# Performance work log

Hardware: AMD Instinct MI355X
Metric: run time of the kernel (lower is better)

The kernel has to match this reference:

```python
import jax, jax.numpy as jnp
import numpy as np
from jax import lax

B, CIN, COUT, H, W, K = 32, 256, 256, 56, 56, 3

def setup_inputs() -> dict:
    key = jax.random.key(0)
    k1, k2, k3 = jax.random.split(key, 3)
    inp = jax.random.normal(k1, (B, CIN, H, W), dtype=jnp.float32)
    # kaiming-style init for conv kernel, normal init for bias
    fan_in = CIN * K * K
    kernel = jax.random.normal(k2, (COUT, CIN, K, K), dtype=jnp.float32) * np.float32(np.sqrt(2.0 / fan_in))
    bias = jax.random.normal(k3, (COUT,), dtype=jnp.float32)
    return {"inp": inp, "kernel": kernel, "bias": bias}

def reference(inp, kernel, bias):
    # Equivalent to the crossbar path: im2col 3x3 patches @ stacked [kernel|bias]
    # matrix == standard conv2d(padding=1, stride=1) + bias.
    out = lax.conv_general_dilated(
        inp, kernel,
        window_strides=(1, 1),
        padding=((1, 1), (1, 1)),
        dimension_numbers=("NCHW", "OIHW", "NCHW"),
    )
    return out + bias[None, :, None, None]
```

## Files before the change

kernel.cpp:

```cpp
#include <hip/hip_runtime.h>
#include <hip/hip_bf16.h>


#define BB    32
#define CINC  256
#define COUTC 256
#define HH    56
#define WW    56
#define HP    58
#define WP    58
#define PIX_PER_IMG 3136
#define NPIX  100352
#define KTOT  2304
#define NKT   72

#define XT_BYTES ((size_t)BB*HP*WP*CINC*2)
#define AWR_FRAGS (72*16*64)
#define AWR_BYTES ((size_t)AWR_FRAGS*16)

#define RING   4096
#define WLDS   (3*RING)

using frag_t = __attribute__((ext_vector_type(8))) short;
using f32x4  = __attribute__((ext_vector_type(4))) float;

__device__ __forceinline__ void gload_lds16(const void* gsrc, void* ldst) {
  __builtin_amdgcn_global_load_lds(
      (const __attribute__((address_space(1))) unsigned*)gsrc,
      (__attribute__((address_space(3))) unsigned*)ldst, 16, 0, 0);
}

__global__ void xpose_kernel(const float* __restrict__ inp,
                             __hip_bfloat16* __restrict__ xt) {
  int bid = blockIdx.x;
  int hp = bid % HP;
  int t  = bid / HP;
  int cb = t % 4;
  int b  = t / 4;
  __shared__ __hip_bfloat16 tile[64 * 60];
  int tid = threadIdx.x;
  for (int i = tid; i < 64 * 60; i += 256) tile[i] = __float2bfloat16(0.f);
  __syncthreads();
  int h = hp - 1;
  if (h >= 0 && h < HH) {
    const float* src = inp + ((size_t)(b * CINC + cb * 64) * HH + h) * WW;
    for (int i = tid; i < 64 * WW; i += 256) {
      int ci = i / WW, w = i - ci * WW;
      tile[ci * 60 + (w + 1)] = __float2bfloat16(src[(size_t)ci * HH * WW + w]);
    }
  }
  __syncthreads();
  __hip_bfloat16* dst = xt + ((size_t)(b * HP + hp) * WP) * CINC + cb * 64;
  for (int i = tid; i < WP * 64; i += 256) {
    int wp = i >> 6, ci = i & 63;
    dst[(size_t)wp * CINC + ci] = tile[ci * 60 + wp];
  }
}

__global__ void wprep_pack(const float* __restrict__ k4,
                           frag_t* __restrict__ awr) {
  int i = blockIdx.x * 256 + threadIdx.x;
  if (i >= AWR_FRAGS) return;
  int lane = i & 63;
  int mb   = (i >> 6) & 15;
  int t    = i >> 10;
  int co   = mb * 16 + (lane & 15);
  int kb   = t * 32 + (lane >> 4) * 8;
  frag_t v;
#pragma unroll
  for (int j = 0; j < 8; ++j) {
    int k = kb + j;
    int tap = k >> 8;
    int ci  = k & 255;
    __hip_bfloat16 h = __float2bfloat16(k4[(co * CINC + ci) * 9 + tap]);
    v[j] = *reinterpret_cast<short*>(&h);
  }
  awr[i] = v;
}

__global__ __launch_bounds__(256, 3) void conv_free(
    const __hip_bfloat16* __restrict__ xt,
    const frag_t* __restrict__ awr,
    const float* __restrict__ bias,
    float* __restrict__ out) {
  __shared__ alignas(16) char lds[4 * WLDS];

  const int tid  = threadIdx.x;
  const int lane = tid & 63;
  const int wid  = tid >> 6;
  const int wm   = wid >> 1;
  const int wn   = wid & 1;
  const int fr   = lane & 15;
  const int g    = lane >> 4;

  const int bid   = blockIdx.x;
  const int wgid  = (bid & 7) * 196 + (bid >> 3);
  const int ctile = wgid & 1;
  const int ptile = wgid >> 1;

  const char* xt_b = (const char*)xt;
  char* wbase = lds + wid * WLDS;

  const int lr  = lane >> 2;
  const int sc  = ((((lane & 3) - ((lane >> 3) & 3)) & 3) << 4);

  auto mkB = [&](int jb) -> const char* {
    int px = ptile * 128 + wn * 64 + jb * 16 + lr;
    int b  = px / PIX_PER_IMG;
    int hw = px - b * PIX_PER_IMG;
    int h = hw / WW, w = hw - h * WW;
    return xt_b + (size_t)((b * HP + h) * WP + w) * (CINC * 2) + sc;
  };
  const char* pB0 = mkB(0);
  const char* pB1 = mkB(1);
  const char* pB2 = mkB(2);
  const char* pB3 = mkB(3);

#define STG(T2, WB) {                                                      \
    int _tap = (T2) >> 3; int _rr = _tap / 3, _ss = _tap - _rr * 3;        \
    size_t _bo = (size_t)(_rr * WP + _ss) * (CINC * 2)                     \
               + (size_t)((T2) & 7) * 64;                                  \
    char* _d = wbase + (WB) * RING;                                        \
    gload_lds16(pB0 + _bo, _d + 0);                                        \
    gload_lds16(pB1 + _bo, _d + 1024);                                     \
    gload_lds16(pB2 + _bo, _d + 2048);                                     \
    gload_lds16(pB3 + _bo, _d + 3072); }

  const frag_t* abase = awr + (size_t)(ctile * 8 + wm * 4) * 64 + lane;

#define ALOAD(T1, FA) {                                                    \
    const frag_t* _p = abase + (size_t)(T1) * (16 * 64);                   \
    _Pragma("unroll") for (int m = 0; m < 4; ++m)                          \
      FA[m] = _p[m * 64]; }

  const int ckr   = (((g + (fr >> 1)) & 3) << 4);
  const int broff = fr * 64 + ckr;

  frag_t fa0[4], fa1[4], fb[4];
  f32x4 acc[4][4] = {};

#define RSL(RB) {                                                          \
    const char* _b = wbase + (RB) * RING;                                  \
    _Pragma("unroll") for (int n = 0; n < 4; ++n)                          \
      fb[n] = *(const frag_t*)(_b + broff + n * 1024); }

#define MF(FA) {                                                           \
    __builtin_amdgcn_s_setprio(1);                                         \
    _Pragma("unroll") for (int m = 0; m < 4; ++m)                          \
    _Pragma("unroll") for (int n = 0; n < 4; ++n)                          \
      acc[m][n] = __builtin_amdgcn_mfma_f32_16x16x32_bf16(                 \
          FA[m], fb[n], acc[m][n], 0, 0, 0);                               \
    __builtin_amdgcn_s_setprio(0); }

#define BODY(T, RB, WB, FCUR, FNXT) {                                      \
    int _t1 = (T) + 1 <= 71 ? (T) + 1 : 71;                                \
    int _t2 = (T) + 2 <= 71 ? (T) + 2 : 71;                                \
    ALOAD(_t1, FNXT);                                                      \
    STG(_t2, WB);                                                          \
    asm volatile("s_waitcnt vmcnt(12)" ::: "memory");                      \
    __builtin_amdgcn_sched_barrier(0);                                     \
    RSL(RB);                                                               \
    MF(FCUR); }

  ALOAD(0, fa0);
  STG(0, 0);
  STG(1, 1);

  for (int base = 0; base < 72; base += 6) {
    BODY(base + 0, 0, 2, fa0, fa1);
    BODY(base + 1, 1, 0, fa1, fa0);
    BODY(base + 2, 2, 1, fa0, fa1);
    BODY(base + 3, 0, 2, fa1, fa0);
    BODY(base + 4, 1, 0, fa0, fa1);
    BODY(base + 5, 2, 1, fa1, fa0);
  }

  int pb[4], phw[4];
#pragma unroll
  for (int n = 0; n < 4; ++n) {
    int pxg = ptile * 128 + wn * 64 + n * 16 + fr;
    pb[n]  = pxg / PIX_PER_IMG;
    phw[n] = pxg - pb[n] * PIX_PER_IMG;
  }
#pragma unroll
  for (int m = 0; m < 4; ++m) {
#pragma unroll
    for (int rg = 0; rg < 4; ++rg) {
      int co = ctile * 128 + wm * 64 + m * 16 + g * 4 + rg;
      float bv = bias[co];
#pragma unroll
      for (int n = 0; n < 4; ++n)
        out[((size_t)pb[n] * COUTC + co) * PIX_PER_IMG + phw[n]] =
            acc[m][n][rg] + bv;
    }
  }
}

__global__ void conv_direct(const float* __restrict__ inp,
                            const float* __restrict__ kern,
                            const float* __restrict__ bias,
                            float* __restrict__ out) {
  int idx = blockIdx.x * 256 + threadIdx.x;
  if (idx >= BB * COUTC * PIX_PER_IMG) return;
  int w = idx % WW;
  int t = idx / WW;
  int h = t % HH; t /= HH;
  int co = t % COUTC;
  int b  = t / COUTC;
  float acc = bias[co];
  for (int ci = 0; ci < CINC; ++ci)
    for (int r = 0; r < 3; ++r) {
      int hh = h + r - 1;
      if (hh < 0 || hh >= HH) continue;
      for (int s = 0; s < 3; ++s) {
        int ww2 = w + s - 1;
        if (ww2 < 0 || ww2 >= WW) continue;
        acc += inp[((size_t)(b * CINC + ci) * HH + hh) * WW + ww2] *
               kern[(co * CINC + ci) * 9 + r * 3 + s];
      }
    }
  out[idx] = acc;
}

extern "C" void kernel_launch(void* const* d_in, const int* in_sizes, int n_in,
                              void* d_out, int out_size, void* d_ws, size_t ws_size,
                              hipStream_t stream) {
  const float* inp  = (const float*)d_in[0];
  const float* kern = (const float*)d_in[1];
  const float* bias = (const float*)d_in[2];
  float* out = (float*)d_out;

  size_t need = XT_BYTES + AWR_BYTES;
  if (ws_size < need) {
    int tot = BB * COUTC * PIX_PER_IMG;
    conv_direct<<<(tot + 255) / 256, 256, 0, stream>>>(inp, kern, bias, out);
    return;
  }

  __hip_bfloat16* xt = (__hip_bfloat16*)d_ws;
  frag_t* awr = (frag_t*)((char*)d_ws + XT_BYTES);

  xpose_kernel<<<BB * 4 * HP, 256, 0, stream>>>(inp, xt);
  wprep_pack<<<(AWR_FRAGS + 255) / 256, 256, 0, stream>>>(kern, awr);
  conv_free<<<2 * (NPIX / 128), 256, 0, stream>>>(xt, awr, bias, out);
}
```

Measured before the change: 219.7 us.

## Load B fragments directly from global into registers, drop LDS staging

The conv kernel no longer stages activation fragments through LDS with global_load_lds. Each lane now loads its B fragments straight from global memory into registers, using a triple-buffered register pipeline two steps ahead for both A and B. Launch bounds drop from 3 to 2 blocks per SIMD to make room for the extra registers, and the explicit waitcnt, sched_barrier and setprio calls are removed. This saves LDS traffic and synchronisation, but loses the LDS swizzle, exposes global memory latency and the compiler's wait placement, and lowers occupancy.

```diff
diff --git a/kernel.cpp b/kernel.cpp
--- a/kernel.cpp
+++ b/kernel.cpp
@@ -18,17 +18,8 @@
 #define AWR_FRAGS (72*16*64)
 #define AWR_BYTES ((size_t)AWR_FRAGS*16)
 
-#define RING   4096
-#define WLDS   (3*RING)
-
 using frag_t = __attribute__((ext_vector_type(8))) short;
 using f32x4  = __attribute__((ext_vector_type(4))) float;
-
-__device__ __forceinline__ void gload_lds16(const void* gsrc, void* ldst) {
-  __builtin_amdgcn_global_load_lds(
-      (const __attribute__((address_space(1))) unsigned*)gsrc,
-      (__attribute__((address_space(3))) unsigned*)ldst, 16, 0, 0);
-}
 
 __global__ void xpose_kernel(const float* __restrict__ inp,
                              __hip_bfloat16* __restrict__ xt) {
@@ -78,13 +69,11 @@
   awr[i] = v;
 }
 
-__global__ __launch_bounds__(256, 3) void conv_free(
+__global__ __launch_bounds__(256, 2) void conv_reg(
     const __hip_bfloat16* __restrict__ xt,
     const frag_t* __restrict__ awr,
     const float* __restrict__ bias,
     float* __restrict__ out) {
-  __shared__ alignas(16) char lds[4 * WLDS];
-
   const int tid  = threadIdx.x;
   const int lane = tid & 63;
   const int wid  = tid >> 6;
@@ -99,80 +88,56 @@
   const int ptile = wgid >> 1;
 
   const char* xt_b = (const char*)xt;
-  char* wbase = lds + wid * WLDS;
-
-  const int lr  = lane >> 2;
-  const int sc  = ((((lane & 3) - ((lane >> 3) & 3)) & 3) << 4);
-
-  auto mkB = [&](int jb) -> const char* {
-    int px = ptile * 128 + wn * 64 + jb * 16 + lr;
+
+  const char* pB[4];
+#pragma unroll
+  for (int n = 0; n < 4; ++n) {
+    int px = ptile * 128 + wn * 64 + n * 16 + fr;
     int b  = px / PIX_PER_IMG;
     int hw = px - b * PIX_PER_IMG;
     int h = hw / WW, w = hw - h * WW;
-    return xt_b + (size_t)((b * HP + h) * WP + w) * (CINC * 2) + sc;
-  };
-  const char* pB0 = mkB(0);
-  const char* pB1 = mkB(1);
-  const char* pB2 = mkB(2);
-  const char* pB3 = mkB(3);
-
-#define STG(T2, WB) {                                                      \
-    int _tap = (T2) >> 3; int _rr = _tap / 3, _ss = _tap - _rr * 3;        \
-    size_t _bo = (size_t)(_rr * WP + _ss) * (CINC * 2)                     \
-               + (size_t)((T2) & 7) * 64;                                  \
-    char* _d = wbase + (WB) * RING;                                        \
-    gload_lds16(pB0 + _bo, _d + 0);                                        \
-    gload_lds16(pB1 + _bo, _d + 1024);                                     \
-    gload_lds16(pB2 + _bo, _d + 2048);                                     \
-    gload_lds16(pB3 + _bo, _d + 3072); }
+    pB[n] = xt_b + (size_t)((b * HP + h) * WP + w) * (CINC * 2) + g * 16;
+  }
 
   const frag_t* abase = awr + (size_t)(ctile * 8 + wm * 4) * 64 + lane;
 
-#define ALOAD(T1, FA) {                                                    \
-    const frag_t* _p = abase + (size_t)(T1) * (16 * 64);                   \
+#define ALOAD(T, FA) {                                                     \
+    const frag_t* _p = abase + (size_t)(T) * 1024;                         \
     _Pragma("unroll") for (int m = 0; m < 4; ++m)                          \
       FA[m] = _p[m * 64]; }
 
-  const int ckr   = (((g + (fr >> 1)) & 3) << 4);
-  const int broff = fr * 64 + ckr;
-
-  frag_t fa0[4], fa1[4], fb[4];
-  f32x4 acc[4][4] = {};
-
-#define RSL(RB) {                                                          \
-    const char* _b = wbase + (RB) * RING;                                  \
+#define BLOAD(T, FB) {                                                     \
+    int _tap = (T) >> 3; int _rr = _tap / 3, _ss = _tap - _rr * 3;         \
+    size_t _bo = (size_t)(_rr * WP + _ss) * (CINC * 2)                     \
+               + (size_t)((T) & 7) * 64;                                   \
     _Pragma("unroll") for (int n = 0; n < 4; ++n)                          \
-      fb[n] = *(const frag_t*)(_b + broff + n * 1024); }
-
-#define MF(FA) {                                                           \
-    __builtin_amdgcn_s_setprio(1);                                         \
+      FB[n] = *(const frag_t*)(pB[n] + _bo); }
+
+#define MF(FA, FB) {                                                       \
     _Pragma("unroll") for (int m = 0; m < 4; ++m)                          \
     _Pragma("unroll") for (int n = 0; n < 4; ++n)                          \
       acc[m][n] = __builtin_amdgcn_mfma_f32_16x16x32_bf16(                 \
-          FA[m], fb[n], acc[m][n], 0, 0, 0);                               \
-    __builtin_amdgcn_s_setprio(0); }
-
-#define BODY(T, RB, WB, FCUR, FNXT) {                                      \
-    int _t1 = (T) + 1 <= 71 ? (T) + 1 : 71;                                \
+          FA[m], FB[n], acc[m][n], 0, 0, 0); }
+
+  frag_t fa0[4], fa1[4], fa2[4], fb0[4], fb1[4], fb2[4];
+  f32x4 acc[4][4] = {};
+
+#define BODY(T, FAc, FBc, FAp, FBp) {                                      \
     int _t2 = (T) + 2 <= 71 ? (T) + 2 : 71;                                \
-    ALOAD(_t1, FNXT);                                                      \
-    STG(_t2, WB);                                                          \
-    asm volatile("s_waitcnt vmcnt(12)" ::: "memory");                      \
-    __builtin_amdgcn_sched_barrier(0);                                     \
-    RSL(RB);                                                               \
-    MF(FCUR); }
-
-  ALOAD(0, fa0);
-  STG(0, 0);
-  STG(1, 1);
+    ALOAD(_t2, FAp);                                                       \
+    BLOAD(_t2, FBp);                                                       \
+    MF(FAc, FBc); }
+
+  ALOAD(0, fa0); BLOAD(0, fb0);
+  ALOAD(1, fa1); BLOAD(1, fb1);
 
   for (int base = 0; base < 72; base += 6) {
-    BODY(base + 0, 0, 2, fa0, fa1);
-    BODY(base + 1, 1, 0, fa1, fa0);
-    BODY(base + 2, 2, 1, fa0, fa1);
-    BODY(base + 3, 0, 2, fa1, fa0);
-    BODY(base + 4, 1, 0, fa0, fa1);
-    BODY(base + 5, 2, 1, fa1, fa0);
+    BODY(base + 0, fa0, fb0, fa2, fb2);
+    BODY(base + 1, fa1, fb1, fa0, fb0);
+    BODY(base + 2, fa2, fb2, fa1, fb1);
+    BODY(base + 3, fa0, fb0, fa2, fb2);
+    BODY(base + 4, fa1, fb1, fa0, fb0);
+    BODY(base + 5, fa2, fb2, fa1, fb1);
   }
 
   int pb[4], phw[4];
@@ -242,5 +207,5 @@
 
   xpose_kernel<<<BB * 4 * HP, 256, 0, stream>>>(inp, xt);
   wprep_pack<<<(AWR_FRAGS + 255) / 256, 256, 0, stream>>>(kern, awr);
-  conv_free<<<2 * (NPIX / 128), 256, 0, stream>>>(xt, awr, bias, out);
-}
+  conv_reg<<<2 * (NPIX / 128), 256, 0, stream>>>(xt, awr, bias, out);
+}
```

Measured after the change: 330.6 us. 1.5x slower.
